# Kernel tuning notes

Measured on AMD Instinct MI355X. Metric: run time of the kernel, lower is better.

The kernel has to match this reference:

```python
import jax, jax.numpy as jnp
import numpy as np

B = 4096
D = 2048
K = 8          # num_intention
H2 = 64        # fc2 out


def setup_inputs() -> dict:
    key = jax.random.key(0)
    ks = jax.random.split(key, 8)
    x = jax.random.normal(ks[0], (B, D), dtype=jnp.float32)
    # one-hot intention per sample
    idx = jax.random.randint(ks[1], (B,), 0, K)
    intention = jax.nn.one_hot(idx, K, dtype=jnp.float32)
    s1 = 1.0 / np.sqrt(D)
    s2 = 1.0 / np.sqrt(K)
    s3 = 1.0 / np.sqrt(D + H2)
    W1 = jax.random.uniform(ks[2], (D * K, D), jnp.float32, -s1, s1)
    b1 = jax.random.uniform(ks[3], (D * K,), jnp.float32, -s1, s1)
    W2 = jax.random.uniform(ks[4], (H2, K), jnp.float32, -s2, s2)
    b2 = jax.random.uniform(ks[5], (H2,), jnp.float32, -s2, s2)
    W3 = jax.random.uniform(ks[6], (1, D + H2), jnp.float32, -s3, s3)
    b3 = jax.random.uniform(ks[7], (1,), jnp.float32, -s3, s3)
    return {"x": x, "intention": intention, "W1": W1, "b1": b1,
            "W2": W2, "b2": b2, "W3": W3, "b3": b3}


def reference(x, intention, W1, b1, W2, b2, W3, b3):
    # fc2 on the one-hot intention -> [B, 64]
    y2 = intention @ W2.T + b2
    # fc1 densely computes all K branches (dropout treated as identity / eval mode)
    y1 = x @ W1.T + b1                      # [B, D*K]
    # mask = intention.repeat(1, 2048): branch axis is INNERMOST (interleaved)
    y1 = y1.reshape(B, D, K)                # [B, D, K]
    sel = jax.lax.stop_gradient(intention)  # mask is non-differentiable in torch
    y1 = jnp.einsum('bdk,bk->bd', y1, sel)  # gather active branch -> [B, D]
    y3 = jax.nn.relu(jnp.concatenate([y1, y2], axis=1))  # [B, D+64]
    y = y3 @ W3.T + b3                      # [B, 1]
    return y
```

## Files before the change

### kernel.cpp

```cpp
#include <hip/hip_runtime.h>
#include <hip/hip_bf16.h>
#include <stdint.h>

#define NB 4096
#define ND 2048
#define NK 8
#define NH 64

#define BM 128
#define BN 128
#define BK 32
#define MAX_ROWS 5120
#define MAX_TILES 40

typedef __bf16 bf16;
typedef __bf16 bf16x8 __attribute__((ext_vector_type(8)));
typedef float floatx4 __attribute__((ext_vector_type(4)));

#define OFF_KIDX   0u
#define OFF_ORDER  16384u
#define OFF_META   40960u
#define OFF_CUR    41472u
#define OFF_C2S    41536u
#define OFF_XG     65536u
#define OFF_WB     21037056u

__global__ void kidx_kernel(const float* __restrict__ intention,
                            int* __restrict__ kidx,
                            int* __restrict__ order)
{
    const int b = blockIdx.x * 256 + threadIdx.x;
    float4 a = *(const float4*)(intention + (size_t)b * NK);
    float4 c = *(const float4*)(intention + (size_t)b * NK + 4);
    int k = 0;
    if (a.y > 0.5f) k = 1;
    if (a.z > 0.5f) k = 2;
    if (a.w > 0.5f) k = 3;
    if (c.x > 0.5f) k = 4;
    if (c.y > 0.5f) k = 5;
    if (c.z > 0.5f) k = 6;
    if (c.w > 0.5f) k = 7;
    kidx[b] = k;
    order[b] = -1;
    if (b < MAX_ROWS - NB) order[NB + b] = -1;
}

__global__ void meta_kernel(const int* __restrict__ kidx,
                            const float* __restrict__ W2,
                            const float* __restrict__ b2,
                            const float* __restrict__ W3,
                            const float* __restrict__ b3,
                            int* __restrict__ meta,
                            int* __restrict__ cursors,
                            float* __restrict__ c2s)
{
    __shared__ int cnt[NK];
    const int tid = threadIdx.x;
    if (tid < NK) cnt[tid] = 0;
    __syncthreads();

    for (int i = tid; i < NB; i += 256)
        atomicAdd(&cnt[kidx[i] & 7], 1);

    if (tid < 64) {
        const int k = tid & 7;
        const int hc = tid >> 3;
        float s = 0.f;
#pragma unroll
        for (int j = 0; j < 8; j++) {
            int h = hc * 8 + j;
            float v = W2[h * NK + k] + b2[h];
            if (v > 0.f) s += v * W3[ND + h];
        }
        s += __shfl_xor(s, 8, 64);
        s += __shfl_xor(s, 16, 64);
        s += __shfl_xor(s, 32, 64);
        if (tid < 8) c2s[k] = s + b3[0];
    }
    __syncthreads();

    if (tid == 0) {
        int running = 0, nt = 0;
        for (int k = 0; k < NK; k++) {
            cursors[k] = running;
            int ntile = (cnt[k] + BM - 1) / BM;
            for (int t = 0; t < ntile && nt < MAX_TILES; t++) {
                meta[1 + nt] = k;
                meta[1 + MAX_TILES + nt] = running + t * BM;
                nt++;
            }
            running += ntile * BM;
        }
        meta[0] = nt;
    }
}

__global__ void scatter_kernel(const int* __restrict__ kidx,
                               int* __restrict__ cursors,
                               const float* __restrict__ c2s,
                               int* __restrict__ order,
                               float* __restrict__ out)
{
    const int b = blockIdx.x * 256 + threadIdx.x;
    const int k = kidx[b] & 7;
    const int pos = atomicAdd(&cursors[k], 1);
    if (pos >= 0 && pos < MAX_ROWS) order[pos] = b;
    out[b] = c2s[k];
}

__global__ void gather_x_kernel(const float* __restrict__ x,
                                const int* __restrict__ order,
                                bf16* __restrict__ xg)
{
    const int row = blockIdx.x;
    const int t = threadIdx.x;
    const int b = order[row];
    bf16* dst = xg + (size_t)row * ND + t * 8;
    bf16x8 v;
    if (b < 0 || b >= NB) {
#pragma unroll
        for (int i = 0; i < 8; i++) v[i] = (bf16)0.f;
    } else {
        const float* src = x + (size_t)b * ND + t * 8;
        float4 a = *(const float4*)(src);
        float4 c = *(const float4*)(src + 4);
        v[0] = (bf16)a.x; v[1] = (bf16)a.y; v[2] = (bf16)a.z; v[3] = (bf16)a.w;
        v[4] = (bf16)c.x; v[5] = (bf16)c.y; v[6] = (bf16)c.z; v[7] = (bf16)c.w;
    }
    *(bf16x8*)dst = v;
}

__global__ void conv_w1_kernel(const float* __restrict__ W1,
                               bf16* __restrict__ Wb)
{
    const int r = blockIdx.x;
    const int t = threadIdx.x;
    const int d = r >> 3;
    const int k = r & 7;
    const float* src = W1 + (size_t)r * ND + t * 8;
    bf16* dst = Wb + ((size_t)k * ND + d) * ND + t * 8;
    float4 a = *(const float4*)(src);
    float4 c = *(const float4*)(src + 4);
    bf16x8 v;
    v[0] = (bf16)a.x; v[1] = (bf16)a.y; v[2] = (bf16)a.z; v[3] = (bf16)a.w;
    v[4] = (bf16)c.x; v[5] = (bf16)c.y; v[6] = (bf16)c.z; v[7] = (bf16)c.w;
    *(bf16x8*)dst = v;
}

__global__ void __launch_bounds__(256)
gemm_kernel(const bf16* __restrict__ xg,
            const bf16* __restrict__ Wb,
            const int* __restrict__ order,
            const int* __restrict__ meta,
            const float* __restrict__ b1,
            const float* __restrict__ W3,
            float* __restrict__ out)
{
    int n_mt = meta[0];
    if (n_mt > MAX_TILES) n_mt = MAX_TILES;
    const int mt = blockIdx.y;
    if (mt >= n_mt) return;
    const int kbr = meta[1 + mt] & 7;
    int row0 = meta[1 + MAX_TILES + mt];
    if (row0 < 0) row0 = 0;
    if (row0 > MAX_ROWS - BM) row0 = MAX_ROWS - BM;
    const int col0 = blockIdx.x * BN;

    __shared__ bf16 As[BM * BK];
    __shared__ bf16 Bs[BN * BK];
    __shared__ int rowb[BM];

    const int tid = threadIdx.x;
    const int lane = tid & 63;
    const int wid = tid >> 6;
    const int wm = wid >> 1;
    const int wn = wid & 1;

    if (tid < BM) rowb[tid] = order[row0 + tid];

    const int fr = lane & 15;
    const int fq = lane >> 4;
    const bf16* gA0 = xg + (size_t)(row0 + wid * 32 + fr) * ND + fq * 8;
    const bf16* gA1 = gA0 + (size_t)16 * ND;
    const bf16* gB0 = Wb + ((size_t)kbr * ND + col0 + wid * 32 + fr) * ND + fq * 8;
    const bf16* gB1 = gB0 + (size_t)16 * ND;
    bf16* lA0 = As + (wid * 2) * 512;
    bf16* lA1 = As + (wid * 2 + 1) * 512;
    bf16* lB0 = Bs + (wid * 2) * 512;
    bf16* lB1 = Bs + (wid * 2 + 1) * 512;

    floatx4 zero = {0.f, 0.f, 0.f, 0.f};
    floatx4 acc[4][4];
#pragma unroll
    for (int i = 0; i < 4; i++)
#pragma unroll
        for (int j = 0; j < 4; j++) acc[i][j] = zero;

    for (int kk = 0; kk < ND; kk += BK) {
        __builtin_amdgcn_global_load_lds(
            (const __attribute__((address_space(1))) void*)(gA0 + kk),
            (__attribute__((address_space(3))) void*)lA0, 16, 0, 0);
        __builtin_amdgcn_global_load_lds(
            (const __attribute__((address_space(1))) void*)(gA1 + kk),
            (__attribute__((address_space(3))) void*)lA1, 16, 0, 0);
        __builtin_amdgcn_global_load_lds(
            (const __attribute__((address_space(1))) void*)(gB0 + kk),
            (__attribute__((address_space(3))) void*)lB0, 16, 0, 0);
        __builtin_amdgcn_global_load_lds(
            (const __attribute__((address_space(1))) void*)(gB1 + kk),
            (__attribute__((address_space(3))) void*)lB1, 16, 0, 0);
        __syncthreads();

        bf16x8 af[4], bfv[4];
#pragma unroll
        for (int i = 0; i < 4; i++) {
            af[i]  = *(const bf16x8*)(As + (wm * 4 + i) * 512 + lane * 8);
            bfv[i] = *(const bf16x8*)(Bs + (wn * 4 + i) * 512 + lane * 8);
        }
#pragma unroll
        for (int i = 0; i < 4; i++)
#pragma unroll
            for (int j = 0; j < 4; j++)
                acc[i][j] = __builtin_amdgcn_mfma_f32_16x16x32_bf16(
                    af[i], bfv[j], acc[i][j], 0, 0, 0);
        __syncthreads();
    }

    const int colq = lane & 15;
    const int quad = lane >> 4;
    float bias[4], w3v[4];
#pragma unroll
    for (int j = 0; j < 4; j++) {
        int d = col0 + wn * 64 + j * 16 + colq;
        bias[j] = b1[d * NK + kbr];
        w3v[j] = W3[d];
    }
#pragma unroll
    for (int i = 0; i < 4; i++) {
#pragma unroll
        for (int r = 0; r < 4; r++) {
            float s = 0.f;
#pragma unroll
            for (int j = 0; j < 4; j++) {
                float v = acc[i][j][r] + bias[j];
                s += (v > 0.f) ? v * w3v[j] : 0.f;
            }
#pragma unroll
            for (int m = 1; m < 16; m <<= 1) s += __shfl_xor(s, m, 64);
            if (colq == 0) {
                int b = rowb[wm * 64 + i * 16 + quad * 4 + r];
                if (b >= 0 && b < NB) atomicAdd(out + b, s);
            }
        }
    }
}

extern "C" void kernel_launch(void* const* d_in, const int* in_sizes, int n_in,
                              void* d_out, int out_size, void* d_ws, size_t ws_size,
                              hipStream_t stream)
{
    const float* x         = (const float*)d_in[0];
    const float* intention = (const float*)d_in[1];
    const float* W1        = (const float*)d_in[2];
    const float* b1        = (const float*)d_in[3];
    const float* W2        = (const float*)d_in[4];
    const float* b2        = (const float*)d_in[5];
    const float* W3        = (const float*)d_in[6];
    const float* b3        = (const float*)d_in[7];
    float* out = (float*)d_out;

    char* ws = (char*)d_ws;
    int*   kidx    = (int*)(ws + OFF_KIDX);
    int*   order   = (int*)(ws + OFF_ORDER);
    int*   meta    = (int*)(ws + OFF_META);
    int*   cursors = (int*)(ws + OFF_CUR);
    float* c2s     = (float*)(ws + OFF_C2S);
    bf16*  xg      = (bf16*)(ws + OFF_XG);
    bf16*  Wb      = (bf16*)(ws + OFF_WB);

    kidx_kernel<<<dim3(16), dim3(256), 0, stream>>>(intention, kidx, order);
    meta_kernel<<<dim3(1), dim3(256), 0, stream>>>(
        kidx, W2, b2, W3, b3, meta, cursors, c2s);
    scatter_kernel<<<dim3(16), dim3(256), 0, stream>>>(
        kidx, cursors, c2s, order, out);
    conv_w1_kernel<<<dim3(NK * ND), dim3(256), 0, stream>>>(W1, Wb);
    gather_x_kernel<<<dim3(MAX_ROWS), dim3(256), 0, stream>>>(x, order, xg);
    gemm_kernel<<<dim3(ND / BN, MAX_TILES), dim3(256), 0, stream>>>(
        xg, Wb, order, meta, b1, W3, out);
}
```

Before: 363.0 us.

## Fuse prep kernels and gather x rows inside GEMM via row indices

Merges W1 conversion, x conversion and intention decoding into one launch, and builds per-block partial histograms so meta no longer rescans kidx. The separate gather kernel is removed: x is converted in original order and the GEMM loads A rows indirectly through the order table. Padding rows are clamped to row 0, with the result discarded at the epilogue. Scatter uses wave-aggregated atomics. This cuts launches and the extra pass over x, at the cost of less contiguous A loads and a changed LDS tile layout that may raise bank conflicts.

Measured after the change: 312.1 us. 1.16x faster.

```diff
diff --git a/kernel.cpp b/kernel.cpp
--- a/kernel.cpp
+++ b/kernel.cpp
@@ -13,6 +13,11 @@
 #define MAX_ROWS 5120
 #define MAX_TILES 40
 
+#define CONV_BLOCKS  (NK * ND)
+#define XCONV_BLOCKS NB
+#define KIDX_BLOCKS  (NB / 256)
+#define PREP_GRID    (CONV_BLOCKS + XCONV_BLOCKS + KIDX_BLOCKS)
+
 typedef __bf16 bf16;
 typedef __bf16 bf16x8 __attribute__((ext_vector_type(8)));
 typedef float floatx4 __attribute__((ext_vector_type(4)));
@@ -22,49 +27,85 @@
 #define OFF_META   40960u
 #define OFF_CUR    41472u
 #define OFF_C2S    41536u
-#define OFF_XG     65536u
-#define OFF_WB     21037056u
-
-__global__ void kidx_kernel(const float* __restrict__ intention,
-                            int* __restrict__ kidx,
-                            int* __restrict__ order)
-{
-    const int b = blockIdx.x * 256 + threadIdx.x;
-    float4 a = *(const float4*)(intention + (size_t)b * NK);
-    float4 c = *(const float4*)(intention + (size_t)b * NK + 4);
-    int k = 0;
-    if (a.y > 0.5f) k = 1;
-    if (a.z > 0.5f) k = 2;
-    if (a.w > 0.5f) k = 3;
-    if (c.x > 0.5f) k = 4;
-    if (c.y > 0.5f) k = 5;
-    if (c.z > 0.5f) k = 6;
-    if (c.w > 0.5f) k = 7;
-    kidx[b] = k;
-    order[b] = -1;
-    if (b < MAX_ROWS - NB) order[NB + b] = -1;
-}
-
-__global__ void meta_kernel(const int* __restrict__ kidx,
-                            const float* __restrict__ W2,
-                            const float* __restrict__ b2,
-                            const float* __restrict__ W3,
-                            const float* __restrict__ b3,
-                            int* __restrict__ meta,
-                            int* __restrict__ cursors,
-                            float* __restrict__ c2s)
+#define OFF_CNTP   41600u
+#define OFF_XC     65536u
+#define OFF_WB     16842752u
+
+__device__ inline void cvt_row16(const float* __restrict__ src, bf16* __restrict__ dst) {
+    float4 a = *(const float4*)(src);
+    float4 c = *(const float4*)(src + 4);
+    bf16x8 v;
+    v[0] = (bf16)a.x; v[1] = (bf16)a.y; v[2] = (bf16)a.z; v[3] = (bf16)a.w;
+    v[4] = (bf16)c.x; v[5] = (bf16)c.y; v[6] = (bf16)c.z; v[7] = (bf16)c.w;
+    *(bf16x8*)dst = v;
+}
+
+__global__ void __launch_bounds__(256)
+prep_conv_kernel(const float* __restrict__ x,
+                 const float* __restrict__ intention,
+                 const float* __restrict__ W1,
+                 int* __restrict__ kidx,
+                 int* __restrict__ cntp,
+                 bf16* __restrict__ xc,
+                 bf16* __restrict__ Wb)
+{
+    const int blk = blockIdx.x;
+    const int tid = threadIdx.x;
+
+    if (blk < CONV_BLOCKS) {
+        const int d = blk >> 3;
+        const int k = blk & 7;
+        cvt_row16(W1 + (size_t)blk * ND + tid * 8,
+                  Wb + ((size_t)k * ND + d) * ND + tid * 8);
+    } else if (blk < CONV_BLOCKS + XCONV_BLOCKS) {
+        const int row = blk - CONV_BLOCKS;
+        cvt_row16(x + (size_t)row * ND + tid * 8,
+                  xc + (size_t)row * ND + tid * 8);
+    } else {
+        __shared__ int h[NK];
+        const int hb = blk - CONV_BLOCKS - XCONV_BLOCKS;
+        if (tid < NK) h[tid] = 0;
+        __syncthreads();
+        const int b = hb * 256 + tid;
+        float4 a = *(const float4*)(intention + (size_t)b * NK);
+        float4 c = *(const float4*)(intention + (size_t)b * NK + 4);
+        int k = 0;
+        if (a.y > 0.5f) k = 1;
+        if (a.z > 0.5f) k = 2;
+        if (a.w > 0.5f) k = 3;
+        if (c.x > 0.5f) k = 4;
+        if (c.y > 0.5f) k = 5;
+        if (c.z > 0.5f) k = 6;
+        if (c.w > 0.5f) k = 7;
+        kidx[b] = k;
+        atomicAdd(&h[k], 1);
+        __syncthreads();
+        if (tid < NK) cntp[hb * NK + tid] = h[tid];
+    }
+}
+
+__global__ void __launch_bounds__(256)
+meta_kernel(const int* __restrict__ cntp,
+            const float* __restrict__ W2,
+            const float* __restrict__ b2,
+            const float* __restrict__ W3,
+            const float* __restrict__ b3,
+            int* __restrict__ meta,
+            int* __restrict__ cursors,
+            float* __restrict__ c2s)
 {
     __shared__ int cnt[NK];
     const int tid = threadIdx.x;
-    if (tid < NK) cnt[tid] = 0;
-    __syncthreads();
-
-    for (int i = tid; i < NB; i += 256)
-        atomicAdd(&cnt[kidx[i] & 7], 1);
-
-    if (tid < 64) {
-        const int k = tid & 7;
-        const int hc = tid >> 3;
+    if (tid < NK) {
+        int s = 0;
+#pragma unroll
+        for (int i = 0; i < KIDX_BLOCKS; i++) s += cntp[i * NK + tid];
+        cnt[tid] = s;
+    }
+    if (tid >= 64 && tid < 128) {
+        const int l = tid - 64;
+        const int k = l & 7;
+        const int hc = l >> 3;
         float s = 0.f;
 #pragma unroll
         for (int j = 0; j < 8; j++) {
@@ -75,10 +116,9 @@
         s += __shfl_xor(s, 8, 64);
         s += __shfl_xor(s, 16, 64);
         s += __shfl_xor(s, 32, 64);
-        if (tid < 8) c2s[k] = s + b3[0];
+        if (l < 8) c2s[k] = s + b3[0];
     }
     __syncthreads();
-
     if (tid == 0) {
         int running = 0, nt = 0;
         for (int k = 0; k < NK; k++) {
@@ -95,60 +135,37 @@
     }
 }
 
-__global__ void scatter_kernel(const int* __restrict__ kidx,
-                               int* __restrict__ cursors,
-                               const float* __restrict__ c2s,
-                               int* __restrict__ order,
-                               float* __restrict__ out)
+__global__ void __launch_bounds__(256)
+scatter_kernel(const int* __restrict__ kidx,
+               int* __restrict__ cursors,
+               const float* __restrict__ c2s,
+               int* __restrict__ order,
+               float* __restrict__ out)
 {
     const int b = blockIdx.x * 256 + threadIdx.x;
+    const int lane = threadIdx.x & 63;
     const int k = kidx[b] & 7;
-    const int pos = atomicAdd(&cursors[k], 1);
+    out[b] = c2s[k];
+
+    const unsigned long long below = (lane == 63) ? ~0ull >> 1
+                                   : ((1ull << lane) - 1);
+    int pos = 0;
+#pragma unroll
+    for (int kk = 0; kk < NK; kk++) {
+        unsigned long long m = __ballot(k == kk);
+        if (m) {
+            int leader = __ffsll((long long)m) - 1;
+            int base = 0;
+            if (lane == leader) base = atomicAdd(&cursors[kk], __popcll(m));
+            base = __shfl(base, leader, 64);
+            if (k == kk) pos = base + __popcll(m & below);
+        }
+    }
     if (pos >= 0 && pos < MAX_ROWS) order[pos] = b;
-    out[b] = c2s[k];
-}
-
-__global__ void gather_x_kernel(const float* __restrict__ x,
-                                const int* __restrict__ order,
-                                bf16* __restrict__ xg)
-{
-    const int row = blockIdx.x;
-    const int t = threadIdx.x;
-    const int b = order[row];
-    bf16* dst = xg + (size_t)row * ND + t * 8;
-    bf16x8 v;
-    if (b < 0 || b >= NB) {
-#pragma unroll
-        for (int i = 0; i < 8; i++) v[i] = (bf16)0.f;
-    } else {
-        const float* src = x + (size_t)b * ND + t * 8;
-        float4 a = *(const float4*)(src);
-        float4 c = *(const float4*)(src + 4);
-        v[0] = (bf16)a.x; v[1] = (bf16)a.y; v[2] = (bf16)a.z; v[3] = (bf16)a.w;
-        v[4] = (bf16)c.x; v[5] = (bf16)c.y; v[6] = (bf16)c.z; v[7] = (bf16)c.w;
-    }
-    *(bf16x8*)dst = v;
-}
-
-__global__ void conv_w1_kernel(const float* __restrict__ W1,
-                               bf16* __restrict__ Wb)
-{
-    const int r = blockIdx.x;
-    const int t = threadIdx.x;
-    const int d = r >> 3;
-    const int k = r & 7;
-    const float* src = W1 + (size_t)r * ND + t * 8;
-    bf16* dst = Wb + ((size_t)k * ND + d) * ND + t * 8;
-    float4 a = *(const float4*)(src);
-    float4 c = *(const float4*)(src + 4);
-    bf16x8 v;
-    v[0] = (bf16)a.x; v[1] = (bf16)a.y; v[2] = (bf16)a.z; v[3] = (bf16)a.w;
-    v[4] = (bf16)c.x; v[5] = (bf16)c.y; v[6] = (bf16)c.z; v[7] = (bf16)c.w;
-    *(bf16x8*)dst = v;
 }
 
 __global__ void __launch_bounds__(256)
-gemm_kernel(const bf16* __restrict__ xg,
+gemm_kernel(const bf16* __restrict__ xc,
             const bf16* __restrict__ Wb,
             const int* __restrict__ order,
             const int* __restrict__ meta,
@@ -176,18 +193,24 @@
     const int wm = wid >> 1;
     const int wn = wid & 1;
 
-    if (tid < BM) rowb[tid] = order[row0 + tid];
-
-    const int fr = lane & 15;
-    const int fq = lane >> 4;
-    const bf16* gA0 = xg + (size_t)(row0 + wid * 32 + fr) * ND + fq * 8;
-    const bf16* gA1 = gA0 + (size_t)16 * ND;
-    const bf16* gB0 = Wb + ((size_t)kbr * ND + col0 + wid * 32 + fr) * ND + fq * 8;
-    const bf16* gB1 = gB0 + (size_t)16 * ND;
-    bf16* lA0 = As + (wid * 2) * 512;
-    bf16* lA1 = As + (wid * 2 + 1) * 512;
-    bf16* lB0 = Bs + (wid * 2) * 512;
-    bf16* lB1 = Bs + (wid * 2 + 1) * 512;
+    if (tid < BM) {
+        int b = order[row0 + tid];
+        rowb[tid] = (b >= 0 && b < NB) ? b : -1;
+    }
+    __syncthreads();
+
+    const int srow = tid >> 2;
+    const int scol = (tid & 3) * 8;
+    const int ra0 = rowb[srow];
+    const int ra1 = rowb[64 + srow];
+    const bf16* pa0 = xc + (size_t)(ra0 < 0 ? 0 : ra0) * ND + scol;
+    const bf16* pa1 = xc + (size_t)(ra1 < 0 ? 0 : ra1) * ND + scol;
+    const bf16* pb0 = Wb + ((size_t)kbr * ND + col0 + srow) * ND + scol;
+    const bf16* pb1 = pb0 + (size_t)64 * ND;
+    bf16* la0 = As + wid * 512;
+    bf16* la1 = As + 2048 + wid * 512;
+    bf16* lb0 = Bs + wid * 512;
+    bf16* lb1 = Bs + 2048 + wid * 512;
 
     floatx4 zero = {0.f, 0.f, 0.f, 0.f};
     floatx4 acc[4][4];
@@ -196,26 +219,29 @@
 #pragma unroll
         for (int j = 0; j < 4; j++) acc[i][j] = zero;
 
+    const int qk = (lane >> 4) * 8;
+    const int mrow = lane & 15;
+
     for (int kk = 0; kk < ND; kk += BK) {
         __builtin_amdgcn_global_load_lds(
-            (const __attribute__((address_space(1))) void*)(gA0 + kk),
-            (__attribute__((address_space(3))) void*)lA0, 16, 0, 0);
+            (const __attribute__((address_space(1))) void*)(pa0 + kk),
+            (__attribute__((address_space(3))) void*)la0, 16, 0, 0);
         __builtin_amdgcn_global_load_lds(
-            (const __attribute__((address_space(1))) void*)(gA1 + kk),
-            (__attribute__((address_space(3))) void*)lA1, 16, 0, 0);
+            (const __attribute__((address_space(1))) void*)(pa1 + kk),
+            (__attribute__((address_space(3))) void*)la1, 16, 0, 0);
         __builtin_amdgcn_global_load_lds(
-            (const __attribute__((address_space(1))) void*)(gB0 + kk),
-            (__attribute__((address_space(3))) void*)lB0, 16, 0, 0);
+            (const __attribute__((address_space(1))) void*)(pb0 + kk),
+            (__attribute__((address_space(3))) void*)lb0, 16, 0, 0);
         __builtin_amdgcn_global_load_lds(
-            (const __attribute__((address_space(1))) void*)(gB1 + kk),
-            (__attribute__((address_space(3))) void*)lB1, 16, 0, 0);
+            (const __attribute__((address_space(1))) void*)(pb1 + kk),
+            (__attribute__((address_space(3))) void*)lb1, 16, 0, 0);
         __syncthreads();
 
         bf16x8 af[4], bfv[4];
 #pragma unroll
         for (int i = 0; i < 4; i++) {
-            af[i]  = *(const bf16x8*)(As + (wm * 4 + i) * 512 + lane * 8);
-            bfv[i] = *(const bf16x8*)(Bs + (wn * 4 + i) * 512 + lane * 8);
+            af[i]  = *(const bf16x8*)(As + (wm * 64 + i * 16 + mrow) * BK + qk);
+            bfv[i] = *(const bf16x8*)(Bs + (wn * 64 + i * 16 + mrow) * BK + qk);
         }
 #pragma unroll
         for (int i = 0; i < 4; i++)
@@ -249,7 +275,7 @@
             for (int m = 1; m < 16; m <<= 1) s += __shfl_xor(s, m, 64);
             if (colq == 0) {
                 int b = rowb[wm * 64 + i * 16 + quad * 4 + r];
-                if (b >= 0 && b < NB) atomicAdd(out + b, s);
+                if (b >= 0) atomicAdd(out + b, s);
             }
         }
     }
@@ -275,16 +301,16 @@
     int*   meta    = (int*)(ws + OFF_META);
     int*   cursors = (int*)(ws + OFF_CUR);
     float* c2s     = (float*)(ws + OFF_C2S);
-    bf16*  xg      = (bf16*)(ws + OFF_XG);
+    int*   cntp    = (int*)(ws + OFF_CNTP);
+    bf16*  xc      = (bf16*)(ws + OFF_XC);
     bf16*  Wb      = (bf16*)(ws + OFF_WB);
 
-    kidx_kernel<<<dim3(16), dim3(256), 0, stream>>>(intention, kidx, order);
+    prep_conv_kernel<<<dim3(PREP_GRID), dim3(256), 0, stream>>>(
+        x, intention, W1, kidx, cntp, xc, Wb);
     meta_kernel<<<dim3(1), dim3(256), 0, stream>>>(
-        kidx, W2, b2, W3, b3, meta, cursors, c2s);
-    scatter_kernel<<<dim3(16), dim3(256), 0, stream>>>(
+        cntp, W2, b2, W3, b3, meta, cursors, c2s);
+    scatter_kernel<<<dim3(NB / 256), dim3(256), 0, stream>>>(
         kidx, cursors, c2s, order, out);
-    conv_w1_kernel<<<dim3(NK * ND), dim3(256), 0, stream>>>(W1, Wb);
-    gather_x_kernel<<<dim3(MAX_ROWS), dim3(256), 0, stream>>>(x, order, xg);
     gemm_kernel<<<dim3(ND / BN, MAX_TILES), dim3(256), 0, stream>>>(
-        xg, Wb, order, meta, b1, W3, out);
-}
+        xc, Wb, order, meta, b1, W3, out);
+}
```
